# Performance work log

Measured on AMD Instinct MI355X. Metric: run time of the kernel, lower is better.

Reference implementation:

```python
import jax, jax.numpy as jnp
import numpy as np

N = 2048

def setup_inputs() -> dict:
    key = jax.random.key(0)
    kx, kq, kk, kv = jax.random.split(key, 4)
    x = jax.random.normal(kx, (N, N), dtype=jnp.float32)
    q = jax.random.normal(kq, (N, N), dtype=jnp.float32)
    k = jax.random.normal(kk, (N, N), dtype=jnp.float32)
    v = jax.random.normal(kv, (N, N), dtype=jnp.float32)
    return {"x": x, "q": q, "k": k, "v": v}

def reference(x, q, k, v):
    # qk = (x @ q) @ (x @ k)  -- note: NOT (x@k).T, faithful to torch.mm chain
    qk = jnp.matmul(jnp.matmul(x, q), jnp.matmul(x, k))  # [n, n]
    attn = jax.nn.softmax(qk, axis=-1)                   # row softmax over n
    return jnp.matmul(attn, jnp.matmul(x, v))            # [n, n]
```

## Files before the change

### kernel.cpp

```cpp
#include <hip/hip_runtime.h>
#include <stdint.h>


#define TN 2048

typedef float f32x4 __attribute__((ext_vector_type(4)));
typedef _Float16 f16;
typedef f16 f16x8 __attribute__((ext_vector_type(8)));
typedef f16 f16x4 __attribute__((ext_vector_type(4)));
typedef unsigned int u32x4 __attribute__((ext_vector_type(4)));

#define MFMA16(a, b, c) __builtin_amdgcn_mfma_f32_16x16x32_f16(a, b, c, 0, 0, 0)

__global__ void split2_kernel(const float* __restrict__ in,
                              f16* __restrict__ t0, f16* __restrict__ t1) {
    int i = (blockIdx.x * 256 + threadIdx.x) * 4;
    f32x4 f = *(const f32x4*)(in + i);
    f16x4 o0, o1;
#pragma unroll
    for (int e = 0; e < 4; ++e) {
        float a = f[e];
        f16 h0 = (f16)a;
        float r = (a - (float)h0) * 4096.f;
        o0[e] = h0; o1[e] = (f16)r;
    }
    *(f16x4*)(t0 + i) = o0; *(f16x4*)(t1 + i) = o1;
}

__global__ void split2_add_kernel(const float* __restrict__ inA,
                                  const float* __restrict__ inB,
                                  f16* __restrict__ t0, f16* __restrict__ t1) {
    int i = (blockIdx.x * 256 + threadIdx.x) * 4;
    f32x4 fa = *(const f32x4*)(inA + i);
    f32x4 fb = *(const f32x4*)(inB + i);
    f16x4 o0, o1;
#pragma unroll
    for (int e = 0; e < 4; ++e) {
        float a = fa[e] + fb[e];
        f16 h0 = (f16)a;
        float r = (a - (float)h0) * 4096.f;
        o0[e] = h0; o1[e] = (f16)r;
    }
    *(f16x4*)(t0 + i) = o0; *(f16x4*)(t1 + i) = o1;
}

__global__ void split2t_kernel(const float* __restrict__ in,
                               f16* __restrict__ t0, f16* __restrict__ t1) {
    __shared__ f16 s0[64][68], s1[64][68];
    int bc = blockIdx.x * 64, br = blockIdx.y * 64;
    int tx = threadIdx.x & 15, ty = threadIdx.x >> 4;
#pragma unroll
    for (int rr = 0; rr < 64; rr += 16) {
        int r = rr + ty;
        f32x4 f = *(const f32x4*)(in + (size_t)(br + r) * TN + bc + tx * 4);
#pragma unroll
        for (int e = 0; e < 4; ++e) {
            float a = f[e];
            f16 h0 = (f16)a;
            float rr2 = (a - (float)h0) * 4096.f;
            s0[tx * 4 + e][r] = h0; s1[tx * 4 + e][r] = (f16)rr2;
        }
    }
    __syncthreads();
#pragma unroll
    for (int rr = 0; rr < 64; rr += 16) {
        int c = rr + ty;
        f16x4 o0, o1;
#pragma unroll
        for (int e = 0; e < 4; ++e) { o0[e] = s0[c][tx*4+e]; o1[e] = s1[c][tx*4+e]; }
        size_t off = (size_t)(bc + c) * TN + br + tx * 4;
        *(f16x4*)(t0 + off) = o0; *(f16x4*)(t1 + off) = o1;
    }
}

__global__ void split2t_add_kernel(const float* __restrict__ inA,
                                   const float* __restrict__ inB,
                                   f16* __restrict__ t0, f16* __restrict__ t1) {
    __shared__ f16 s0[64][68], s1[64][68];
    int bc = blockIdx.x * 64, br = blockIdx.y * 64;
    int tx = threadIdx.x & 15, ty = threadIdx.x >> 4;
#pragma unroll
    for (int rr = 0; rr < 64; rr += 16) {
        int r = rr + ty;
        size_t off = (size_t)(br + r) * TN + bc + tx * 4;
        f32x4 fa = *(const f32x4*)(inA + off);
        f32x4 fb = *(const f32x4*)(inB + off);
#pragma unroll
        for (int e = 0; e < 4; ++e) {
            float a = fa[e] + fb[e];
            f16 h0 = (f16)a;
            float rr2 = (a - (float)h0) * 4096.f;
            s0[tx * 4 + e][r] = h0; s1[tx * 4 + e][r] = (f16)rr2;
        }
    }
    __syncthreads();
#pragma unroll
    for (int rr = 0; rr < 64; rr += 16) {
        int c = rr + ty;
        f16x4 o0, o1;
#pragma unroll
        for (int e = 0; e < 4; ++e) { o0[e] = s0[c][tx*4+e]; o1[e] = s1[c][tx*4+e]; }
        size_t off = (size_t)(bc + c) * TN + br + tx * 4;
        *(f16x4*)(t0 + off) = o0; *(f16x4*)(t1 + off) = o1;
    }
}

__global__ void cast1t_kernel(const float* __restrict__ in, f16* __restrict__ t0) {
    __shared__ f16 s0[64][68];
    int bc = blockIdx.x * 64, br = blockIdx.y * 64;
    int tx = threadIdx.x & 15, ty = threadIdx.x >> 4;
#pragma unroll
    for (int rr = 0; rr < 64; rr += 16) {
        int r = rr + ty;
        f32x4 f = *(const f32x4*)(in + (size_t)(br + r) * TN + bc + tx * 4);
#pragma unroll
        for (int e = 0; e < 4; ++e) s0[tx * 4 + e][r] = (f16)f[e];
    }
    __syncthreads();
#pragma unroll
    for (int rr = 0; rr < 64; rr += 16) {
        int c = rr + ty;
        f16x4 o0;
#pragma unroll
        for (int e = 0; e < 4; ++e) o0[e] = s0[c][tx*4+e];
        *(f16x4*)(t0 + (size_t)(bc + c) * TN + br + tx * 4) = o0;
    }
}

__global__ void cast1t_add_kernel(const float* __restrict__ inA,
                                  const float* __restrict__ inB,
                                  f16* __restrict__ t0) {
    __shared__ f16 s0[64][68];
    int bc = blockIdx.x * 64, br = blockIdx.y * 64;
    int tx = threadIdx.x & 15, ty = threadIdx.x >> 4;
#pragma unroll
    for (int rr = 0; rr < 64; rr += 16) {
        int r = rr + ty;
        size_t off = (size_t)(br + r) * TN + bc + tx * 4;
        f32x4 fa = *(const f32x4*)(inA + off);
        f32x4 fb = *(const f32x4*)(inB + off);
#pragma unroll
        for (int e = 0; e < 4; ++e) s0[tx * 4 + e][r] = (f16)(fa[e] + fb[e]);
    }
    __syncthreads();
#pragma unroll
    for (int rr = 0; rr < 64; rr += 16) {
        int c = rr + ty;
        f16x4 o0;
#pragma unroll
        for (int e = 0; e < 4; ++e) o0[e] = s0[c][tx*4+e];
        *(f16x4*)(t0 + (size_t)(bc + c) * TN + br + tx * 4) = o0;
    }
}

__global__ void final_add_kernel(const float* __restrict__ inA,
                                 const float* __restrict__ inB,
                                 float* __restrict__ out) {
    int i = (blockIdx.x * 256 + threadIdx.x) * 4;
    f32x4 fa = *(const f32x4*)(inA + i);
    f32x4 fb = *(const f32x4*)(inB + i);
    f32x4 o;
#pragma unroll
    for (int e = 0; e < 4; ++e) o[e] = fa[e] + fb[e];
    *(f32x4*)(out + i) = o;
}

__global__ __launch_bounds__(256, 2) void gemm3_f16(
    const f16* __restrict__ a0p, const f16* __restrict__ a1p,
    const f16* __restrict__ b0p, const f16* __restrict__ b1p,
    float* __restrict__ C0, float* __restrict__ C1) {
    __shared__ f16 lds[2][32 * 512];
    const int tid = threadIdx.x;
    const int wave = tid >> 6, lane = tid & 63;
    const int wr = (wave >> 1) * 64, wc = (wave & 1) * 64;
    const int quad = lane >> 4, l16 = lane & 15;
    const int bm = blockIdx.y * 128, bn = blockIdx.x * 128;
    const int kbase = blockIdx.z * 1024;
    float* __restrict__ C = blockIdx.z ? C1 : C0;

    const f16* sp[8];
#pragma unroll
    for (int t = 0; t < 8; ++t) {
        int s = wave * 8 + t;
        const f16* base; int gr;
        if (s < 16) { base = (s & 8) ? a1p : a0p; gr = bm + (s & 7) * 16 + l16; }
        else        { base = (s & 8) ? b1p : b0p; gr = bn + (s & 7) * 16 + l16; }
        sp[t] = base + (size_t)gr * TN + kbase + quad * 8;
    }
    const int dof = wave * 8 * 512 + lane * 8;
    const int rof = lane * 8;

    f32x4 acc1[4][4], acc2[4][4];
#pragma unroll
    for (int i = 0; i < 4; ++i)
#pragma unroll
        for (int j = 0; j < 4; ++j) {
            acc1[i][j] = (f32x4){0.f, 0.f, 0.f, 0.f};
            acc2[i][j] = (f32x4){0.f, 0.f, 0.f, 0.f};
        }

    u32x4 g[8];
#pragma unroll
    for (int t = 0; t < 8; ++t) { g[t] = *(const u32x4*)sp[t]; sp[t] += 32; }
#pragma unroll
    for (int t = 0; t < 8; ++t) *(u32x4*)(&lds[0][0] + dof + t * 512) = g[t];
#pragma unroll
    for (int t = 0; t < 8; ++t) { g[t] = *(const u32x4*)sp[t]; sp[t] += 32; }

    for (int step = 0; step < 32; ++step) {
        const int p = step & 1;
        __syncthreads();
        const f16* rdb = &lds[p][0] + rof;
        f16x8 b0f[4], b1f[4], a0f[4], a1f[4];
#pragma unroll
        for (int j = 0; j < 4; ++j) {
            b0f[j] = *(const f16x8*)(rdb + (16 + (wc >> 4) + j) * 512);
            b1f[j] = *(const f16x8*)(rdb + (24 + (wc >> 4) + j) * 512);
        }
#pragma unroll
        for (int i = 0; i < 4; ++i) {
            a0f[i] = *(const f16x8*)(rdb + ((wr >> 4) + i) * 512);
            a1f[i] = *(const f16x8*)(rdb + (8 + (wr >> 4) + i) * 512);
        }
        if (step < 31) {
            f16* dst = &lds[1 - p][0] + dof;
#pragma unroll
            for (int t = 0; t < 8; ++t) *(u32x4*)(dst + t * 512) = g[t];
        }
        if (step < 30) {
#pragma unroll
            for (int t = 0; t < 8; ++t) { g[t] = *(const u32x4*)sp[t]; sp[t] += 32; }
        }
#pragma unroll
        for (int i = 0; i < 4; ++i)
#pragma unroll
            for (int j = 0; j < 4; ++j) {
                acc1[i][j] = MFMA16(a0f[i], b0f[j], acc1[i][j]);
                acc2[i][j] = MFMA16(a0f[i], b1f[j], acc2[i][j]);
                acc2[i][j] = MFMA16(a1f[i], b0f[j], acc2[i][j]);
            }
    }
    const float sc = 1.f / 4096.f;
#pragma unroll
    for (int i = 0; i < 4; ++i)
#pragma unroll
        for (int j = 0; j < 4; ++j) {
            int row = bm + wr + i * 16 + quad * 4;
            int col = bn + wc + j * 16 + l16;
            float* p = C + (size_t)row * TN + col;
#pragma unroll
            for (int r = 0; r < 4; ++r)
                p[(size_t)r * TN] = acc1[i][j][r] + acc2[i][j][r] * sc;
        }
}

__global__ __launch_bounds__(256, 2) void gemm1_f16(
    const f16* __restrict__ A, const f16* __restrict__ Bt,
    float* __restrict__ C0, float* __restrict__ C1) {
    __shared__ f16 lds[2][16 * 512];
    const int tid = threadIdx.x;
    const int wave = tid >> 6, lane = tid & 63;
    const int wr = (wave >> 1) * 64, wc = (wave & 1) * 64;
    const int quad = lane >> 4, l16 = lane & 15;
    const int bm = blockIdx.y * 128, bn = blockIdx.x * 128;
    const int kbase = blockIdx.z * 1024;
    float* __restrict__ C = blockIdx.z ? C1 : C0;

    const f16* sp[4];
#pragma unroll
    for (int t = 0; t < 4; ++t) {
        int s = wave * 4 + t;
        const f16* base; int gr;
        if (s < 8) { base = A;  gr = bm + s * 16 + l16; }
        else       { base = Bt; gr = bn + (s - 8) * 16 + l16; }
        sp[t] = base + (size_t)gr * TN + kbase + quad * 8;
    }
    const int dof = wave * 4 * 512 + lane * 8;
    const int rof = lane * 8;

    f32x4 acc[4][4];
#pragma unroll
    for (int i = 0; i < 4; ++i)
#pragma unroll
        for (int j = 0; j < 4; ++j) acc[i][j] = (f32x4){0.f, 0.f, 0.f, 0.f};

    u32x4 g[4];
#pragma unroll
    for (int t = 0; t < 4; ++t) { g[t] = *(const u32x4*)sp[t]; sp[t] += 32; }
#pragma unroll
    for (int t = 0; t < 4; ++t) *(u32x4*)(&lds[0][0] + dof + t * 512) = g[t];
#pragma unroll
    for (int t = 0; t < 4; ++t) { g[t] = *(const u32x4*)sp[t]; sp[t] += 32; }

    for (int step = 0; step < 32; ++step) {
        const int p = step & 1;
        __syncthreads();
        const f16* rdb = &lds[p][0] + rof;
        f16x8 bf[4], af[4];
#pragma unroll
        for (int j = 0; j < 4; ++j) bf[j] = *(const f16x8*)(rdb + (8 + (wc >> 4) + j) * 512);
#pragma unroll
        for (int i = 0; i < 4; ++i) af[i] = *(const f16x8*)(rdb + ((wr >> 4) + i) * 512);
        if (step < 31) {
            f16* dst = &lds[1 - p][0] + dof;
#pragma unroll
            for (int t = 0; t < 4; ++t) *(u32x4*)(dst + t * 512) = g[t];
        }
        if (step < 30) {
#pragma unroll
            for (int t = 0; t < 4; ++t) { g[t] = *(const u32x4*)sp[t]; sp[t] += 32; }
        }
#pragma unroll
        for (int i = 0; i < 4; ++i)
#pragma unroll
            for (int j = 0; j < 4; ++j) acc[i][j] = MFMA16(af[i], bf[j], acc[i][j]);
    }
#pragma unroll
    for (int i = 0; i < 4; ++i)
#pragma unroll
        for (int j = 0; j < 4; ++j) {
            int row = bm + wr + i * 16 + quad * 4;
            int col = bn + wc + j * 16 + l16;
            float* p = C + (size_t)row * TN + col;
#pragma unroll
            for (int r = 0; r < 4; ++r) p[(size_t)r * TN] = acc[i][j][r];
        }
}

__global__ void softmax_add_kernel(const float* __restrict__ S0,
                                   const float* __restrict__ S1,
                                   f16* __restrict__ P) {
    __shared__ float red[256];
    const int row = blockIdx.x, tid = threadIdx.x;
    const size_t base = (size_t)row * TN + tid * 8;
    f32x4 a0 = *(const f32x4*)(S0 + base);
    f32x4 a1 = *(const f32x4*)(S0 + base + 4);
    f32x4 b0 = *(const f32x4*)(S1 + base);
    f32x4 b1 = *(const f32x4*)(S1 + base + 4);
    float vals[8];
#pragma unroll
    for (int e = 0; e < 4; ++e) { vals[e] = a0[e] + b0[e]; vals[4 + e] = a1[e] + b1[e]; }
    float m = vals[0];
#pragma unroll
    for (int e = 1; e < 8; ++e) m = fmaxf(m, vals[e]);
    red[tid] = m; __syncthreads();
    for (int st = 128; st > 0; st >>= 1) { if (tid < st) red[tid] = fmaxf(red[tid], red[tid + st]); __syncthreads(); }
    m = red[0]; __syncthreads();
    float sum = 0.f;
#pragma unroll
    for (int e = 0; e < 8; ++e) { vals[e] = expf(vals[e] - m); sum += vals[e]; }
    red[tid] = sum; __syncthreads();
    for (int st = 128; st > 0; st >>= 1) { if (tid < st) red[tid] += red[tid + st]; __syncthreads(); }
    float inv = 1.f / red[0];
    f16x8 o;
#pragma unroll
    for (int e = 0; e < 8; ++e) o[e] = (f16)(vals[e] * inv);
    *(f16x8*)(P + base) = o;
}

extern "C" void kernel_launch(void* const* d_in, const int* in_sizes, int n_in,
                              void* d_out, int out_size, void* d_ws, size_t ws_size,
                              hipStream_t stream) {
    const float* x = (const float*)d_in[0];
    const float* q = (const float*)d_in[1];
    const float* k = (const float*)d_in[2];
    const float* v = (const float*)d_in[3];
    float* out = (float*)d_out;
    const size_t M = (size_t)TN * TN;

    float* W1 = (float*)d_ws;
    float* W2 = W1 + M;
    f16* pl = (f16*)(W2 + M);
    f16 *x0 = pl,         *x1 = pl + M;
    f16 *q0 = pl + 2 * M, *q1 = pl + 3 * M;
    f16 *k0 = pl + 4 * M, *k1 = pl + 5 * M;
    f16 *v0 = pl + 6 * M;
    f16 *a0 = q0, *a1 = q1;
    f16 *b0 = k0, *b1 = k1;
    f16 *p0 = x1, *c0 = x0;

    dim3 bs(256);
    dim3 gelem(TN * TN / 4 / 256);
    dim3 gt(TN / 64, TN / 64);
    dim3 gg(TN / 128, TN / 128, 2);

    hipLaunchKernelGGL(split2_kernel,  gelem, bs, 0, stream, x, x0, x1);
    hipLaunchKernelGGL(cast1t_kernel,  gt,    bs, 0, stream, v, v0);
    hipLaunchKernelGGL(split2t_kernel, gt,    bs, 0, stream, q, q0, q1);
    hipLaunchKernelGGL(gemm3_f16, gg, bs, 0, stream, x0, x1, q0, q1, W1, W2);
    hipLaunchKernelGGL(split2_add_kernel, gelem, bs, 0, stream, W1, W2, a0, a1);
    hipLaunchKernelGGL(split2t_kernel, gt, bs, 0, stream, k, k0, k1);
    hipLaunchKernelGGL(gemm3_f16, gg, bs, 0, stream, x0, x1, k0, k1, W1, W2);
    hipLaunchKernelGGL(split2t_add_kernel, gt, bs, 0, stream, W1, W2, b0, b1);
    hipLaunchKernelGGL(gemm3_f16, gg, bs, 0, stream, a0, a1, b0, b1, W1, W2);
    hipLaunchKernelGGL(softmax_add_kernel, dim3(TN), bs, 0, stream, W1, W2, p0);
    hipLaunchKernelGGL(gemm1_f16, gg, bs, 0, stream, x0, v0, W1, W2);
    hipLaunchKernelGGL(cast1t_add_kernel, gt, bs, 0, stream, W1, W2, c0);
    hipLaunchKernelGGL(gemm1_f16, gg, bs, 0, stream, p0, c0, W1, W2);
    hipLaunchKernelGGL(final_add_kernel, gelem, bs, 0, stream, W1, W2, out);
}
```

Measured before the change: 423.2 us.

## Pipeline GEMMs with direct global-to-LDS loads and triple buffering

Both f16 GEMM kernels now load tiles straight into LDS with global_load_lds and use a three-stage buffer ring. The loop synchronizes with raw s_barrier/vmcnt waits and raises wave priority around the MFMA blocks. gemm3 becomes a 512-thread, 128x256 tile kernel that accumulates all three split products into one accumulator. The residual split drops its 4096 scaling, so the low part is stored unscaled in f16. This aims to hide global load latency and cut register staging and the epilogue. The risk is precision loss: unscaled residuals can fall into the f16 subnormal range. The hand-written barriers also make ordering fragile, and LDS use per block grows.

```diff
diff --git a/kernel.cpp b/kernel.cpp
--- a/kernel.cpp
+++ b/kernel.cpp
@@ -8,9 +8,16 @@
 typedef _Float16 f16;
 typedef f16 f16x8 __attribute__((ext_vector_type(8)));
 typedef f16 f16x4 __attribute__((ext_vector_type(4)));
-typedef unsigned int u32x4 __attribute__((ext_vector_type(4)));
 
 #define MFMA16(a, b, c) __builtin_amdgcn_mfma_f32_16x16x32_f16(a, b, c, 0, 0, 0)
+#define SBAR() asm volatile("s_barrier" ::: "memory")
+#define VMCNT(n) asm volatile("s_waitcnt vmcnt(" #n ")" ::: "memory")
+
+__device__ __forceinline__ void glds16(const f16* g, f16* l) {
+    __builtin_amdgcn_global_load_lds(
+        (const __attribute__((address_space(1))) unsigned int*)g,
+        (__attribute__((address_space(3))) unsigned int*)l, 16, 0, 0);
+}
 
 __global__ void split2_kernel(const float* __restrict__ in,
                               f16* __restrict__ t0, f16* __restrict__ t1) {
@@ -21,8 +28,7 @@
     for (int e = 0; e < 4; ++e) {
         float a = f[e];
         f16 h0 = (f16)a;
-        float r = (a - (float)h0) * 4096.f;
-        o0[e] = h0; o1[e] = (f16)r;
+        o0[e] = h0; o1[e] = (f16)(a - (float)h0);
     }
     *(f16x4*)(t0 + i) = o0; *(f16x4*)(t1 + i) = o1;
 }
@@ -38,8 +44,7 @@
     for (int e = 0; e < 4; ++e) {
         float a = fa[e] + fb[e];
         f16 h0 = (f16)a;
-        float r = (a - (float)h0) * 4096.f;
-        o0[e] = h0; o1[e] = (f16)r;
+        o0[e] = h0; o1[e] = (f16)(a - (float)h0);
     }
     *(f16x4*)(t0 + i) = o0; *(f16x4*)(t1 + i) = o1;
 }
@@ -57,8 +62,7 @@
         for (int e = 0; e < 4; ++e) {
             float a = f[e];
             f16 h0 = (f16)a;
-            float rr2 = (a - (float)h0) * 4096.f;
-            s0[tx * 4 + e][r] = h0; s1[tx * 4 + e][r] = (f16)rr2;
+            s0[tx * 4 + e][r] = h0; s1[tx * 4 + e][r] = (f16)(a - (float)h0);
         }
     }
     __syncthreads();
@@ -89,8 +93,7 @@
         for (int e = 0; e < 4; ++e) {
             float a = fa[e] + fb[e];
             f16 h0 = (f16)a;
-            float rr2 = (a - (float)h0) * 4096.f;
-            s0[tx * 4 + e][r] = h0; s1[tx * 4 + e][r] = (f16)rr2;
+            s0[tx * 4 + e][r] = h0; s1[tx * 4 + e][r] = (f16)(a - (float)h0);
         }
     }
     __syncthreads();
@@ -165,11 +168,113 @@
     *(f32x4*)(out + i) = o;
 }
 
-__global__ __launch_bounds__(256, 2) void gemm3_f16(
+__global__ __launch_bounds__(512, 2) void gemm3_f16(
     const f16* __restrict__ a0p, const f16* __restrict__ a1p,
     const f16* __restrict__ b0p, const f16* __restrict__ b1p,
     float* __restrict__ C0, float* __restrict__ C1) {
-    __shared__ f16 lds[2][32 * 512];
+    __shared__ f16 lds[3][48 * 512];
+    const int tid = threadIdx.x;
+    const int wave = tid >> 6, lane = tid & 63;
+    const int wrow = wave >> 2, wcol = wave & 3;
+    const int quad = lane >> 4, l16 = lane & 15;
+    const int bm = blockIdx.y * 128, bn = blockIdx.x * 256;
+    const int kbase = blockIdx.z * 1024;
+    float* __restrict__ C = blockIdx.z ? C1 : C0;
+
+    const int ws = wave * 6;
+    const f16* sp[6];
+#pragma unroll
+    for (int t = 0; t < 6; ++t) {
+        int s = ws + t;
+        const f16* base; int gr;
+        if (s < 8)       { base = a0p; gr = bm + s * 16 + l16; }
+        else if (s < 16) { base = a1p; gr = bm + (s - 8) * 16 + l16; }
+        else if (s < 32) { base = b0p; gr = bn + (s - 16) * 16 + l16; }
+        else             { base = b1p; gr = bn + (s - 32) * 16 + l16; }
+        sp[t] = base + (size_t)gr * TN + kbase + quad * 8;
+    }
+    const int rof = lane * 8;
+    const int sa0 = wrow * 4, sa1 = 8 + wrow * 4;
+    const int sb0 = 16 + wcol * 4, sb1 = 32 + wcol * 4;
+
+    f32x4 acc[4][4];
+#pragma unroll
+    for (int i = 0; i < 4; ++i)
+#pragma unroll
+        for (int j = 0; j < 4; ++j) acc[i][j] = (f32x4){0.f, 0.f, 0.f, 0.f};
+
+#pragma unroll
+    for (int t = 0; t < 6; ++t) { glds16(sp[t], &lds[0][(ws + t) * 512]); sp[t] += 32; }
+#pragma unroll
+    for (int t = 0; t < 6; ++t) { glds16(sp[t], &lds[1][(ws + t) * 512]); sp[t] += 32; }
+    f16* cur = &lds[0][0]; f16* nxt = &lds[1][0]; f16* pre = &lds[2][0];
+    VMCNT(6); SBAR();
+
+    f16x8 a0f[4], a1f[4], b0f[4], b1f[4];
+#pragma unroll
+    for (int i = 0; i < 4; ++i) a0f[i] = *(const f16x8*)(cur + (sa0 + i) * 512 + rof);
+#pragma unroll
+    for (int j = 0; j < 4; ++j) b0f[j] = *(const f16x8*)(cur + (sb0 + j) * 512 + rof);
+
+    for (int step = 0; step < 32; ++step) {
+#pragma unroll
+        for (int j = 0; j < 4; ++j) b1f[j] = *(const f16x8*)(cur + (sb1 + j) * 512 + rof);
+        if (step < 30) {
+#pragma unroll
+            for (int t = 0; t < 3; ++t) { glds16(sp[t], pre + (ws + t) * 512); sp[t] += 32; }
+        }
+        SBAR();
+        __builtin_amdgcn_s_setprio(1);
+#pragma unroll
+        for (int i = 0; i < 4; ++i)
+#pragma unroll
+            for (int j = 0; j < 4; ++j) acc[i][j] = MFMA16(a0f[i], b0f[j], acc[i][j]);
+        __builtin_amdgcn_s_setprio(0);
+#pragma unroll
+        for (int i = 0; i < 4; ++i) a1f[i] = *(const f16x8*)(cur + (sa1 + i) * 512 + rof);
+        if (step < 30) {
+#pragma unroll
+            for (int t = 3; t < 6; ++t) { glds16(sp[t], pre + (ws + t) * 512); sp[t] += 32; }
+        }
+        SBAR();
+        __builtin_amdgcn_s_setprio(1);
+#pragma unroll
+        for (int i = 0; i < 4; ++i)
+#pragma unroll
+            for (int j = 0; j < 4; ++j) acc[i][j] = MFMA16(a0f[i], b1f[j], acc[i][j]);
+        __builtin_amdgcn_s_setprio(0);
+        __builtin_amdgcn_s_setprio(1);
+#pragma unroll
+        for (int i = 0; i < 4; ++i)
+#pragma unroll
+            for (int j = 0; j < 4; ++j) acc[i][j] = MFMA16(a1f[i], b0f[j], acc[i][j]);
+        __builtin_amdgcn_s_setprio(0);
+        if (step < 31) {
+            if (step < 30) { VMCNT(6); } else { VMCNT(0); }
+            SBAR();
+#pragma unroll
+            for (int i = 0; i < 4; ++i) a0f[i] = *(const f16x8*)(nxt + (sa0 + i) * 512 + rof);
+#pragma unroll
+            for (int j = 0; j < 4; ++j) b0f[j] = *(const f16x8*)(nxt + (sb0 + j) * 512 + rof);
+        }
+        f16* tmp = cur; cur = nxt; nxt = pre; pre = tmp;
+    }
+#pragma unroll
+    for (int i = 0; i < 4; ++i)
+#pragma unroll
+        for (int j = 0; j < 4; ++j) {
+            int row = bm + wrow * 64 + i * 16 + quad * 4;
+            int col = bn + wcol * 64 + j * 16 + l16;
+            float* p = C + (size_t)row * TN + col;
+#pragma unroll
+            for (int r = 0; r < 4; ++r) p[(size_t)r * TN] = acc[i][j][r];
+        }
+}
+
+__global__ __launch_bounds__(256, 2) void gemm1_f16(
+    const f16* __restrict__ A, const f16* __restrict__ Bt,
+    float* __restrict__ C0, float* __restrict__ C1) {
+    __shared__ f16 lds[3][16 * 512];
     const int tid = threadIdx.x;
     const int wave = tid >> 6, lane = tid & 63;
     const int wr = (wave >> 1) * 64, wc = (wave & 1) * 64;
@@ -178,105 +283,18 @@
     const int kbase = blockIdx.z * 1024;
     float* __restrict__ C = blockIdx.z ? C1 : C0;
 
-    const f16* sp[8];
-#pragma unroll
-    for (int t = 0; t < 8; ++t) {
-        int s = wave * 8 + t;
-        const f16* base; int gr;
-        if (s < 16) { base = (s & 8) ? a1p : a0p; gr = bm + (s & 7) * 16 + l16; }
-        else        { base = (s & 8) ? b1p : b0p; gr = bn + (s & 7) * 16 + l16; }
-        sp[t] = base + (size_t)gr * TN + kbase + quad * 8;
-    }
-    const int dof = wave * 8 * 512 + lane * 8;
-    const int rof = lane * 8;
-
-    f32x4 acc1[4][4], acc2[4][4];
-#pragma unroll
-    for (int i = 0; i < 4; ++i)
-#pragma unroll
-        for (int j = 0; j < 4; ++j) {
-            acc1[i][j] = (f32x4){0.f, 0.f, 0.f, 0.f};
-            acc2[i][j] = (f32x4){0.f, 0.f, 0.f, 0.f};
-        }
-
-    u32x4 g[8];
-#pragma unroll
-    for (int t = 0; t < 8; ++t) { g[t] = *(const u32x4*)sp[t]; sp[t] += 32; }
-#pragma unroll
-    for (int t = 0; t < 8; ++t) *(u32x4*)(&lds[0][0] + dof + t * 512) = g[t];
-#pragma unroll
-    for (int t = 0; t < 8; ++t) { g[t] = *(const u32x4*)sp[t]; sp[t] += 32; }
-
-    for (int step = 0; step < 32; ++step) {
-        const int p = step & 1;
-        __syncthreads();
-        const f16* rdb = &lds[p][0] + rof;
-        f16x8 b0f[4], b1f[4], a0f[4], a1f[4];
-#pragma unroll
-        for (int j = 0; j < 4; ++j) {
-            b0f[j] = *(const f16x8*)(rdb + (16 + (wc >> 4) + j) * 512);
-            b1f[j] = *(const f16x8*)(rdb + (24 + (wc >> 4) + j) * 512);
-        }
-#pragma unroll
-        for (int i = 0; i < 4; ++i) {
-            a0f[i] = *(const f16x8*)(rdb + ((wr >> 4) + i) * 512);
-            a1f[i] = *(const f16x8*)(rdb + (8 + (wr >> 4) + i) * 512);
-        }
-        if (step < 31) {
-            f16* dst = &lds[1 - p][0] + dof;
-#pragma unroll
-            for (int t = 0; t < 8; ++t) *(u32x4*)(dst + t * 512) = g[t];
-        }
-        if (step < 30) {
-#pragma unroll
-            for (int t = 0; t < 8; ++t) { g[t] = *(const u32x4*)sp[t]; sp[t] += 32; }
-        }
-#pragma unroll
-        for (int i = 0; i < 4; ++i)
-#pragma unroll
-            for (int j = 0; j < 4; ++j) {
-                acc1[i][j] = MFMA16(a0f[i], b0f[j], acc1[i][j]);
-                acc2[i][j] = MFMA16(a0f[i], b1f[j], acc2[i][j]);
-                acc2[i][j] = MFMA16(a1f[i], b0f[j], acc2[i][j]);
-            }
-    }
-    const float sc = 1.f / 4096.f;
-#pragma unroll
-    for (int i = 0; i < 4; ++i)
-#pragma unroll
-        for (int j = 0; j < 4; ++j) {
-            int row = bm + wr + i * 16 + quad * 4;
-            int col = bn + wc + j * 16 + l16;
-            float* p = C + (size_t)row * TN + col;
-#pragma unroll
-            for (int r = 0; r < 4; ++r)
-                p[(size_t)r * TN] = acc1[i][j][r] + acc2[i][j][r] * sc;
-        }
-}
-
-__global__ __launch_bounds__(256, 2) void gemm1_f16(
-    const f16* __restrict__ A, const f16* __restrict__ Bt,
-    float* __restrict__ C0, float* __restrict__ C1) {
-    __shared__ f16 lds[2][16 * 512];
-    const int tid = threadIdx.x;
-    const int wave = tid >> 6, lane = tid & 63;
-    const int wr = (wave >> 1) * 64, wc = (wave & 1) * 64;
-    const int quad = lane >> 4, l16 = lane & 15;
-    const int bm = blockIdx.y * 128, bn = blockIdx.x * 128;
-    const int kbase = blockIdx.z * 1024;
-    float* __restrict__ C = blockIdx.z ? C1 : C0;
-
+    const int ws = wave * 4;
     const f16* sp[4];
 #pragma unroll
     for (int t = 0; t < 4; ++t) {
-        int s = wave * 4 + t;
+        int s = ws + t;
         const f16* base; int gr;
         if (s < 8) { base = A;  gr = bm + s * 16 + l16; }
         else       { base = Bt; gr = bn + (s - 8) * 16 + l16; }
         sp[t] = base + (size_t)gr * TN + kbase + quad * 8;
     }
-    const int dof = wave * 4 * 512 + lane * 8;
     const int rof = lane * 8;
+    const int sa = (wr >> 4), sb = 8 + (wc >> 4);
 
     f32x4 acc[4][4];
 #pragma unroll
@@ -284,36 +302,40 @@
 #pragma unroll
         for (int j = 0; j < 4; ++j) acc[i][j] = (f32x4){0.f, 0.f, 0.f, 0.f};
 
-    u32x4 g[4];
-#pragma unroll
-    for (int t = 0; t < 4; ++t) { g[t] = *(const u32x4*)sp[t]; sp[t] += 32; }
-#pragma unroll
-    for (int t = 0; t < 4; ++t) *(u32x4*)(&lds[0][0] + dof + t * 512) = g[t];
-#pragma unroll
-    for (int t = 0; t < 4; ++t) { g[t] = *(const u32x4*)sp[t]; sp[t] += 32; }
+#pragma unroll
+    for (int t = 0; t < 4; ++t) { glds16(sp[t], &lds[0][(ws + t) * 512]); sp[t] += 32; }
+#pragma unroll
+    for (int t = 0; t < 4; ++t) { glds16(sp[t], &lds[1][(ws + t) * 512]); sp[t] += 32; }
+    f16* cur = &lds[0][0]; f16* nxt = &lds[1][0]; f16* pre = &lds[2][0];
+    VMCNT(4); SBAR();
+
+    f16x8 af[4], bf[4];
+#pragma unroll
+    for (int i = 0; i < 4; ++i) af[i] = *(const f16x8*)(cur + (sa + i) * 512 + rof);
+#pragma unroll
+    for (int j = 0; j < 4; ++j) bf[j] = *(const f16x8*)(cur + (sb + j) * 512 + rof);
 
     for (int step = 0; step < 32; ++step) {
-        const int p = step & 1;
-        __syncthreads();
-        const f16* rdb = &lds[p][0] + rof;
-        f16x8 bf[4], af[4];
-#pragma unroll
-        for (int j = 0; j < 4; ++j) bf[j] = *(const f16x8*)(rdb + (8 + (wc >> 4) + j) * 512);
-#pragma unroll
-        for (int i = 0; i < 4; ++i) af[i] = *(const f16x8*)(rdb + ((wr >> 4) + i) * 512);
+        if (step < 30) {
+#pragma unroll
+            for (int t = 0; t < 4; ++t) { glds16(sp[t], pre + (ws + t) * 512); sp[t] += 32; }
+        }
+        SBAR();
+        __builtin_amdgcn_s_setprio(1);
+#pragma unroll
+        for (int i = 0; i < 4; ++i)
+#pragma unroll
+            for (int j = 0; j < 4; ++j) acc[i][j] = MFMA16(af[i], bf[j], acc[i][j]);
+        __builtin_amdgcn_s_setprio(0);
         if (step < 31) {
-            f16* dst = &lds[1 - p][0] + dof;
-#pragma unroll
-            for (int t = 0; t < 4; ++t) *(u32x4*)(dst + t * 512) = g[t];
-        }
-        if (step < 30) {
-#pragma unroll
-            for (int t = 0; t < 4; ++t) { g[t] = *(const u32x4*)sp[t]; sp[t] += 32; }
-        }
-#pragma unroll
-        for (int i = 0; i < 4; ++i)
-#pragma unroll
-            for (int j = 0; j < 4; ++j) acc[i][j] = MFMA16(af[i], bf[j], acc[i][j]);
+            if (step < 30) { VMCNT(4); } else { VMCNT(0); }
+            SBAR();
+#pragma unroll
+            for (int i = 0; i < 4; ++i) af[i] = *(const f16x8*)(nxt + (sa + i) * 512 + rof);
+#pragma unroll
+            for (int j = 0; j < 4; ++j) bf[j] = *(const f16x8*)(nxt + (sb + j) * 512 + rof);
+        }
+        f16* tmp = cur; cur = nxt; nxt = pre; pre = tmp;
     }
 #pragma unroll
     for (int i = 0; i < 4; ++i)
@@ -379,23 +401,24 @@
     f16 *b0 = k0, *b1 = k1;
     f16 *p0 = x1, *c0 = x0;
 
-    dim3 bs(256);
+    dim3 bs(256), bs3(512);
     dim3 gelem(TN * TN / 4 / 256);
     dim3 gt(TN / 64, TN / 64);
-    dim3 gg(TN / 128, TN / 128, 2);
+    dim3 gg3(TN / 256, TN / 128, 2);
+    dim3 gg1(TN / 128, TN / 128, 2);
 
     hipLaunchKernelGGL(split2_kernel,  gelem, bs, 0, stream, x, x0, x1);
     hipLaunchKernelGGL(cast1t_kernel,  gt,    bs, 0, stream, v, v0);
     hipLaunchKernelGGL(split2t_kernel, gt,    bs, 0, stream, q, q0, q1);
-    hipLaunchKernelGGL(gemm3_f16, gg, bs, 0, stream, x0, x1, q0, q1, W1, W2);
+    hipLaunchKernelGGL(gemm3_f16, gg3, bs3, 0, stream, x0, x1, q0, q1, W1, W2);
     hipLaunchKernelGGL(split2_add_kernel, gelem, bs, 0, stream, W1, W2, a0, a1);
     hipLaunchKernelGGL(split2t_kernel, gt, bs, 0, stream, k, k0, k1);
-    hipLaunchKernelGGL(gemm3_f16, gg, bs, 0, stream, x0, x1, k0, k1, W1, W2);
+    hipLaunchKernelGGL(gemm3_f16, gg3, bs3, 0, stream, x0, x1, k0, k1, W1, W2);
     hipLaunchKernelGGL(split2t_add_kernel, gt, bs, 0, stream, W1, W2, b0, b1);
-    hipLaunchKernelGGL(gemm3_f16, gg, bs, 0, stream, a0, a1, b0, b1, W1, W2);
+    hipLaunchKernelGGL(gemm3_f16, gg3, bs3, 0, stream, a0, a1, b0, b1, W1, W2);
     hipLaunchKernelGGL(softmax_add_kernel, dim3(TN), bs, 0, stream, W1, W2, p0);
-    hipLaunchKernelGGL(gemm1_f16, gg, bs, 0, stream, x0, v0, W1, W2);
+    hipLaunchKernelGGL(gemm1_f16, gg1, bs, 0, stream, x0, v0, W1, W2);
     hipLaunchKernelGGL(cast1t_add_kernel, gt, bs, 0, stream, W1, W2, c0);
-    hipLaunchKernelGGL(gemm1_f16, gg, bs, 0, stream, p0, c0, W1, W2);
+    hipLaunchKernelGGL(gemm1_f16, gg1, bs, 0, stream, p0, c0, W1, W2);
     hipLaunchKernelGGL(final_add_kernel, gelem, bs, 0, stream, W1, W2, out);
 }
```

Measured after the change: 390.8 us. 7.7% less time.
